# Kernel tuning notes

Measured on AMD Instinct MI355X. Metric: run time of the kernel, lower is better.

Reference implementation:

```python
import jax, jax.numpy as jnp
import numpy as np

HEAD = 8
KERNEL = 7


def setup_inputs() -> dict:
    key = jax.random.key(0)
    ks = jax.random.split(key, 5)
    N, C, H, W = 2, 256, 56, 56
    scale = 1.0 / np.sqrt(C)
    queries = jax.random.normal(ks[0], (N, C, H, W), jnp.float32)
    key_t = jax.random.normal(ks[1], (N, C, H, W), jnp.float32)
    in_proj_w = jax.random.normal(ks[2], (3 * C, C), jnp.float32) * scale
    in_proj_b = jnp.zeros((3 * C,), jnp.float32)
    out_proj_w = jax.random.normal(ks[3], (C, C), jnp.float32) * scale
    out_proj_b = jnp.zeros((C,), jnp.float32)
    pos_enc = jnp.full((1, 1), float(KERNEL ** 2), jnp.float32)  # nn.Parameter([[kernel**2]])
    return dict(queries=queries, key=key_t, pos_enc=pos_enc,
                in_proj_w=in_proj_w, in_proj_b=in_proj_b,
                out_proj_w=out_proj_w, out_proj_b=out_proj_b)


def reference(queries, key, pos_enc, in_proj_w, in_proj_b, out_proj_w, out_proj_b):
    N, C, H, W = queries.shape
    k2 = KERNEL * KERNEL
    c = (KERNEL - 1) // 2
    # zero-pad key and extract k x k neighborhoods (same ordering as unfold: row-major i*k+j)
    kp = jnp.pad(key, ((0, 0), (0, 0), (c, c), (c, c)))
    patches = jnp.stack([kp[:, :, i:i + H, j:j + W]
                         for i in range(KERNEL) for j in range(KERNEL)], axis=-1)  # (N,C,H,W,k2)
    kv = patches.reshape(N, C, H * W, k2) + pos_enc[0, 0]   # scalar position bias
    kv = kv.transpose(0, 2, 3, 1)                            # (N, P, k2, C), P = H*W pixels
    q = queries.reshape(N, C, H * W).transpose(0, 2, 1)      # (N, P, C)

    Wq, Wk, Wv = jnp.split(in_proj_w, 3, axis=0)
    bq, bk, bv = jnp.split(in_proj_b, 3)
    d = C // HEAD
    qh = (q @ Wq.T + bq).reshape(N, H * W, HEAD, d)
    kh = (kv @ Wk.T + bk).reshape(N, H * W, k2, HEAD, d)
    vh = (kv @ Wv.T + bv).reshape(N, H * W, k2, HEAD, d)

    scores = jnp.einsum('nphd,npkhd->nphk', qh, kh) / jnp.sqrt(jnp.asarray(d, qh.dtype))
    attn = jax.nn.softmax(scores, axis=-1)
    o = jnp.einsum('nphk,npkhd->nphd', attn, vh).reshape(N, H * W, C)
    out = o @ out_proj_w.T + out_proj_b                       # (N, P, C)
    return out.transpose(0, 2, 1).reshape(N, C, H, W)
```

## Files before the change

kernel.cpp:

```cpp
#include <hip/hip_runtime.h>
#include <stdint.h>

#define HW 56
#define P 3136
#define C 256
#define CP (C*P)

typedef float  f32x4  __attribute__((ext_vector_type(4)));
typedef short  short8 __attribute__((ext_vector_type(8)));

__device__ __forceinline__ unsigned short f2bf(float f) {
    uint32_t u = __float_as_uint(f);
    uint32_t r = (u + 0x7fffu + ((u >> 16) & 1u)) >> 16;
    return (unsigned short)r;
}
__device__ __forceinline__ float bl(uint32_t u) { return __uint_as_float(u << 16); }
__device__ __forceinline__ float bh(uint32_t u) { return __uint_as_float(u & 0xffff0000u); }

__device__ __forceinline__ void gload16(const void* g, const void* l) {
    __builtin_amdgcn_global_load_lds(
        (const __attribute__((address_space(1))) uint32_t*)g,
        (__attribute__((address_space(3))) uint32_t*)l, 16, 0, 0);
}

__global__ __launch_bounds__(256) void wconv_vb_kernel(const float* __restrict__ ipw,
                                                       const float* __restrict__ opw,
                                                       const float* __restrict__ ipb,
                                                       const float* __restrict__ pos,
                                                       unsigned short* __restrict__ Wb,
                                                       float* __restrict__ vbc) {
    int bx = blockIdx.x;
    if (bx < 256) {
        int i4 = bx * 256 + threadIdx.x;
        const float4* src = (i4 < 49152) ? (const float4*)ipw : (const float4*)opw;
        int idx = (i4 < 49152) ? i4 : i4 - 49152;
        float4 v = src[idx];
        ((ushort4*)Wb)[i4] = make_ushort4(f2bf(v.x), f2bf(v.y), f2bf(v.z), f2bf(v.w));
    } else {
        int b = bx - 256;
        int w = threadIdx.x >> 6, lane = threadIdx.x & 63;
        float pe = pos[0];
        #pragma unroll
        for (int i = 0; i < 4; ++i) {
            int r = b * 16 + w * 4 + i;
            const float* row = ipw + (size_t)(512 + r) * 256;
            float s = row[lane] + row[lane + 64] + row[lane + 128] + row[lane + 192];
            #pragma unroll
            for (int off = 32; off; off >>= 1) s += __shfl_xor(s, off);
            if (lane == 0) vbc[r] = fmaf(pe, s, ipb[512 + r]);
        }
    }
}

__global__ __launch_bounds__(256) void tconv_kernel(const float* __restrict__ queries,
                                                    const float* __restrict__ key,
                                                    unsigned short* __restrict__ Qt,
                                                    unsigned short* __restrict__ Kt) {
    __shared__ float Ls[64][65];
    int t = threadIdx.x;
    int p0 = blockIdx.x * 64, ci0 = blockIdx.y * 64;
    int n = blockIdx.z & 1, which = blockIdx.z >> 1;
    const float* X = (which ? key : queries) + (size_t)n * CP;
    unsigned short* Xt = (which ? Kt : Qt) + (size_t)n * P * 256;

    int c = t & 63, r0 = t >> 6;
    #pragma unroll
    for (int rr = 0; rr < 16; ++rr) {
        int cil = r0 * 16 + rr;
        Ls[c][cil] = X[(size_t)(ci0 + cil) * P + p0 + c];
    }
    __syncthreads();
    int pl = t >> 2, cch = (t & 3) * 16;
    uint32_t us[8];
    #pragma unroll
    for (int j = 0; j < 8; ++j) {
        float lo = Ls[pl][cch + 2 * j], hi = Ls[pl][cch + 2 * j + 1];
        us[j] = (uint32_t)f2bf(lo) | ((uint32_t)f2bf(hi) << 16);
    }
    uint4* dst = (uint4*)(Xt + (size_t)(p0 + pl) * 256 + ci0 + cch);
    dst[0] = make_uint4(us[0], us[1], us[2], us[3]);
    dst[1] = make_uint4(us[4], us[5], us[6], us[7]);
}

__device__ __forceinline__ void gemm_core(const unsigned short* __restrict__ A,
                                          const unsigned short* __restrict__ B,
                                          int p0, unsigned short* As, unsigned short* Bs,
                                          f32x4 acc[4][2]) {
    int tid = threadIdx.x;
    int wid = __builtin_amdgcn_readfirstlane(tid >> 6);
    int lane = tid & 63;
    int wr = wid >> 1, wc = wid & 1;

    #pragma unroll
    for (int m = 0; m < 4; ++m)
        #pragma unroll
        for (int j = 0; j < 2; ++j) acc[m][j] = (f32x4){0.f, 0.f, 0.f, 0.f};

    for (int k0 = 0; k0 < 256; k0 += 32) {
        #pragma unroll
        for (int i = 0; i < 2; ++i) {
            int ch = i * 256 + (wid << 6) + lane;
            int row = ch >> 2;
            int g = (ch & 3) ^ ((row >> 1) & 3);
            gload16(A + (size_t)row * 256 + k0 + g * 8, (const char*)As + i * 4096 + wid * 1024);
        }
        {
            int ch = (wid << 6) + lane;
            int row = ch >> 2;
            int g = (ch & 3) ^ ((row >> 1) & 3);
            gload16(B + (size_t)(p0 + row) * 256 + k0 + g * 8, (const char*)Bs + wid * 1024);
        }
        __syncthreads();
        short8 af[4], bfr[2];
        #pragma unroll
        for (int m = 0; m < 4; ++m) {
            int col = (wr << 6) + m * 16 + (lane & 15);
            int phys = (lane >> 4) ^ ((col >> 1) & 3);
            af[m] = *(const short8*)((const char*)As + col * 64 + phys * 16);
        }
        #pragma unroll
        for (int j = 0; j < 2; ++j) {
            int pl = (wc << 5) + j * 16 + (lane & 15);
            int phys = (lane >> 4) ^ ((pl >> 1) & 3);
            bfr[j] = *(const short8*)((const char*)Bs + pl * 64 + phys * 16);
        }
        #pragma unroll
        for (int m = 0; m < 4; ++m)
            #pragma unroll
            for (int j = 0; j < 2; ++j)
                acc[m][j] = __builtin_amdgcn_mfma_f32_16x16x32_bf16(af[m], bfr[j], acc[m][j], 0, 0, 0);
        __syncthreads();
    }
}

__global__ __launch_bounds__(256) void proj_mfma(const unsigned short* __restrict__ Wb,
                                                 const unsigned short* __restrict__ Qt,
                                                 const unsigned short* __restrict__ Kt,
                                                 const float* __restrict__ ipb,
                                                 unsigned short* __restrict__ Qb,
                                                 unsigned short* __restrict__ Kb,
                                                 unsigned short* __restrict__ Vb) {
    __shared__ __align__(16) unsigned short As[4096];
    __shared__ __align__(16) unsigned short Bs[2048];
    int ty = blockIdx.y, n = blockIdx.z;
    int p0 = blockIdx.x * 64;
    int proj = ty >> 1;
    int co0 = ty * 128;
    const unsigned short* A = Wb + (size_t)co0 * 256;
    const unsigned short* B = (proj == 0 ? Qt : Kt) + (size_t)n * P * 256;
    unsigned short* outb = (proj == 0 ? Qb : (proj == 1 ? Kb : Vb)) + (size_t)n * 8 * P * 32;
    int col0 = (ty & 1) * 128;

    f32x4 acc[4][2];
    gemm_core(A, B, p0, As, Bs, acc);

    int lane = threadIdx.x & 63;
    int wid = threadIdx.x >> 6;
    int wr = wid >> 1, wc = wid & 1;
    #pragma unroll
    for (int m = 0; m < 4; ++m)
        #pragma unroll
        for (int j = 0; j < 2; ++j) {
            int col = col0 + (wr << 6) + m * 16 + (lane >> 4) * 4;
            int p   = p0 + (wc << 5) + j * 16 + (lane & 15);
            float v0 = acc[m][j][0], v1 = acc[m][j][1], v2 = acc[m][j][2], v3 = acc[m][j][3];
            if (proj == 0) {
                int cg = co0 + (wr << 6) + m * 16 + (lane >> 4) * 4;
                v0 += ipb[cg]; v1 += ipb[cg + 1]; v2 += ipb[cg + 2]; v3 += ipb[cg + 3];
            }
            int h = col >> 5, d = col & 31;
            ushort4 u = make_ushort4(f2bf(v0), f2bf(v1), f2bf(v2), f2bf(v3));
            *(ushort4*)(outb + ((size_t)(h * P + p)) * 32 + d) = u;
        }
}

__constant__ const float kScale = 0.17677669529663687f;

template<int T0, int T1>
__device__ __forceinline__ void tap_range(const float* __restrict__ q,
                                          const unsigned short* __restrict__ Kbase,
                                          int p, int y, int x,
                                          float* __restrict__ ws_col, float& l) {
    #pragma unroll
    for (int t = T0; t < T1; ++t) {
        int dy = t / 7 - 3, dx = t % 7 - 3;
        int yy = y + dy, xx = x + dx;
        bool in = (yy >= 0) & (yy < HW) & (xx >= 0) & (xx < HW);
        int pnb = in ? (p + dy * HW + dx) : p;
        const uint4* kr = (const uint4*)(Kbase + (size_t)pnb * 32);
        float dot = 0.f;
        #pragma unroll
        for (int c = 0; c < 4; ++c) {
            uint4 u = kr[c];
            dot = fmaf(q[c*8+0], bl(u.x), dot); dot = fmaf(q[c*8+1], bh(u.x), dot);
            dot = fmaf(q[c*8+2], bl(u.y), dot); dot = fmaf(q[c*8+3], bh(u.y), dot);
            dot = fmaf(q[c*8+4], bl(u.z), dot); dot = fmaf(q[c*8+5], bh(u.z), dot);
            dot = fmaf(q[c*8+6], bl(u.w), dot); dot = fmaf(q[c*8+7], bh(u.w), dot);
        }
        float e = in ? __expf(dot * kScale) : 0.f;
        l += in ? e : 1.0f;
        ws_col[t * 64] = e;
    }
}

__global__ __launch_bounds__(256) void attn_kernel(const unsigned short* __restrict__ Qb,
                                                   const unsigned short* __restrict__ Kb,
                                                   const unsigned short* __restrict__ Vb,
                                                   unsigned short* __restrict__ Ot) {
    __shared__ float Ws[49][64];
    __shared__ float Lp[4][64];
    int tid = threadIdx.x;
    int lane = tid & 63, wave = tid >> 6;
    int p = blockIdx.x * 64 + lane;
    int h = blockIdx.y, n = blockIdx.z;
    int y = p / HW, x = p % HW;

    const unsigned short* Kbase = Kb + (size_t)(n * 8 + h) * P * 32;
    const unsigned short* Vbase = Vb + (size_t)(n * 8 + h) * P * 32;

    const uint4* qr = (const uint4*)(Qb + ((size_t)((n * 8 + h) * P + p)) * 32);
    float q[32];
    #pragma unroll
    for (int c = 0; c < 4; ++c) {
        uint4 u = qr[c];
        q[c*8+0] = bl(u.x); q[c*8+1] = bh(u.x); q[c*8+2] = bl(u.y); q[c*8+3] = bh(u.y);
        q[c*8+4] = bl(u.z); q[c*8+5] = bh(u.z); q[c*8+6] = bl(u.w); q[c*8+7] = bh(u.w);
    }

    float l = 0.f;
    float* ws_col = &Ws[0][lane];
    if      (wave == 0) tap_range< 0, 13>(q, Kbase, p, y, x, ws_col, l);
    else if (wave == 1) tap_range<13, 25>(q, Kbase, p, y, x, ws_col, l);
    else if (wave == 2) tap_range<25, 37>(q, Kbase, p, y, x, ws_col, l);
    else                tap_range<37, 49>(q, Kbase, p, y, x, ws_col, l);
    Lp[wave][lane] = l;
    __syncthreads();

    float lt = Lp[0][lane] + Lp[1][lane] + Lp[2][lane] + Lp[3][lane];
    float inv = __builtin_amdgcn_rcpf(lt);

    int d0 = wave * 8;
    float o[8] = {0.f, 0.f, 0.f, 0.f, 0.f, 0.f, 0.f, 0.f};
    #pragma unroll
    for (int t = 0; t < 49; ++t) {
        int dy = t / 7 - 3, dx = t % 7 - 3;
        int yy = y + dy, xx = x + dx;
        bool in = (yy >= 0) & (yy < HW) & (xx >= 0) & (xx < HW);
        int pnb = in ? (p + dy * HW + dx) : p;
        float w = Ws[t][lane];
        uint4 u = *(const uint4*)(Vbase + (size_t)pnb * 32 + d0);
        o[0] = fmaf(w, bl(u.x), o[0]); o[1] = fmaf(w, bh(u.x), o[1]);
        o[2] = fmaf(w, bl(u.y), o[2]); o[3] = fmaf(w, bh(u.y), o[3]);
        o[4] = fmaf(w, bl(u.z), o[4]); o[5] = fmaf(w, bh(u.z), o[5]);
        o[6] = fmaf(w, bl(u.w), o[6]); o[7] = fmaf(w, bh(u.w), o[7]);
    }
    uint32_t us[4];
    #pragma unroll
    for (int j = 0; j < 4; ++j)
        us[j] = (uint32_t)f2bf(o[2*j] * inv) | ((uint32_t)f2bf(o[2*j+1] * inv) << 16);
    *(uint4*)(Ot + (size_t)(n * P + p) * 256 + h * 32 + d0) =
        make_uint4(us[0], us[1], us[2], us[3]);
}

__global__ __launch_bounds__(256) void outproj_mfma(const unsigned short* __restrict__ Wb,
                                                    const unsigned short* __restrict__ Ot,
                                                    const float* __restrict__ opw,
                                                    const float* __restrict__ opb,
                                                    const float* __restrict__ vbc,
                                                    float* __restrict__ out) {
    __shared__ __align__(16) unsigned short As[4096];
    __shared__ __align__(16) unsigned short Bs[2048];
    __shared__ float obc_s[128];
    int tid = threadIdx.x;
    int n = blockIdx.z;
    int p0 = blockIdx.x * 64;
    int co0 = blockIdx.y * 128;

    {
        int r = tid >> 1, half = tid & 1;
        const float* row = opw + (size_t)(co0 + r) * 256 + half * 128;
        const float* vh = vbc + half * 128;
        float s = 0.f;
        #pragma unroll 8
        for (int i = 0; i < 128; ++i) s = fmaf(row[i], vh[i], s);
        s += __shfl_xor(s, 1);
        if (half == 0) obc_s[r] = s + opb[co0 + r];
    }

    const unsigned short* A = Wb + (size_t)(768 + co0) * 256;
    const unsigned short* B = Ot + (size_t)n * P * 256;
    f32x4 acc[4][2];
    gemm_core(A, B, p0, As, Bs, acc);

    int lane = tid & 63;
    int wid = tid >> 6;
    int wr = wid >> 1, wc = wid & 1;
    #pragma unroll
    for (int m = 0; m < 4; ++m)
        #pragma unroll
        for (int j = 0; j < 2; ++j) {
            int col = (wr << 6) + m * 16 + (lane >> 4) * 4;
            int p  = p0 + (wc << 5) + j * 16 + (lane & 15);
            #pragma unroll
            for (int i = 0; i < 4; ++i)
                out[(size_t)n * CP + (size_t)(co0 + col + i) * P + p] = acc[m][j][i] + obc_s[col + i];
        }
}

extern "C" void kernel_launch(void* const* d_in, const int* in_sizes, int n_in,
                              void* d_out, int out_size, void* d_ws, size_t ws_size,
                              hipStream_t stream) {
    (void)in_sizes; (void)n_in; (void)out_size; (void)ws_size;
    const float* queries = (const float*)d_in[0];
    const float* key     = (const float*)d_in[1];
    const float* pos     = (const float*)d_in[2];
    const float* ipw     = (const float*)d_in[3];
    const float* ipb     = (const float*)d_in[4];
    const float* opw     = (const float*)d_in[5];
    const float* opb     = (const float*)d_in[6];
    float* out = (float*)d_out;

    unsigned short* us = (unsigned short*)d_ws;
    const size_t SZ = (size_t)2 * P * 256;
    unsigned short* Qt = us;
    unsigned short* Kt = us + SZ;
    unsigned short* Qb = us + 2 * SZ;
    unsigned short* Kb = us + 3 * SZ;
    unsigned short* Vb = us + 4 * SZ;
    unsigned short* Ot = us + 5 * SZ;
    unsigned short* Wb = us + 6 * SZ;
    float* vbc = (float*)(us + 6 * SZ + 262144);

    hipLaunchKernelGGL(wconv_vb_kernel, dim3(272), dim3(256), 0, stream,
                       ipw, opw, ipb, pos, Wb, vbc);
    hipLaunchKernelGGL(tconv_kernel, dim3(49, 4, 4), dim3(256), 0, stream,
                       queries, key, Qt, Kt);
    hipLaunchKernelGGL(proj_mfma, dim3(49, 6, 2), dim3(256), 0, stream,
                       Wb, Qt, Kt, ipb, Qb, Kb, Vb);
    hipLaunchKernelGGL(attn_kernel, dim3(49, 8, 2), dim3(256), 0, stream, Qb, Kb, Vb, Ot);
    hipLaunchKernelGGL(outproj_mfma, dim3(49, 2, 2), dim3(256), 0, stream,
                       Wb, Ot, opw, opb, vbc, out);
}
```

Baseline: 126.5 us.

## Merge prep kernels, deepen GEMM K-step to 64, shrink outproj tile

Folds the weight-conversion and transpose-convert kernels into a single prep launch, removing one kernel launch and its serialization. The shared GEMM core now loads K=64 per iteration with an 8-way XOR swizzle, halving the number of barrier pairs per tile. The output projection uses 64-row output tiles instead of 128, doubling its block count for better CU occupancy on a small grid. This costs more LDS per block in the projection kernel and more redundant bias-vector work in outproj.

Result: faster. 122.0 us, median of 2 (-3.6%).

```diff
diff --git a/kernel.cpp b/kernel.cpp
--- a/kernel.cpp
+++ b/kernel.cpp
@@ -23,12 +23,17 @@
         (__attribute__((address_space(3))) uint32_t*)l, 16, 0, 0);
 }
 
-__global__ __launch_bounds__(256) void wconv_vb_kernel(const float* __restrict__ ipw,
-                                                       const float* __restrict__ opw,
-                                                       const float* __restrict__ ipb,
-                                                       const float* __restrict__ pos,
-                                                       unsigned short* __restrict__ Wb,
-                                                       float* __restrict__ vbc) {
+__global__ __launch_bounds__(256) void prep_kernel(const float* __restrict__ queries,
+                                                   const float* __restrict__ key,
+                                                   const float* __restrict__ ipw,
+                                                   const float* __restrict__ opw,
+                                                   const float* __restrict__ ipb,
+                                                   const float* __restrict__ pos,
+                                                   unsigned short* __restrict__ Wb,
+                                                   float* __restrict__ vbc,
+                                                   unsigned short* __restrict__ Qt,
+                                                   unsigned short* __restrict__ Kt) {
+    __shared__ float Ls[64][65];
     int bx = blockIdx.x;
     if (bx < 256) {
         int i4 = bx * 256 + threadIdx.x;
@@ -36,7 +41,7 @@
         int idx = (i4 < 49152) ? i4 : i4 - 49152;
         float4 v = src[idx];
         ((ushort4*)Wb)[i4] = make_ushort4(f2bf(v.x), f2bf(v.y), f2bf(v.z), f2bf(v.w));
-    } else {
+    } else if (bx < 272) {
         int b = bx - 256;
         int w = threadIdx.x >> 6, lane = threadIdx.x & 63;
         float pe = pos[0];
@@ -49,86 +54,92 @@
             for (int off = 32; off; off >>= 1) s += __shfl_xor(s, off);
             if (lane == 0) vbc[r] = fmaf(pe, s, ipb[512 + r]);
         }
-    }
-}
-
-__global__ __launch_bounds__(256) void tconv_kernel(const float* __restrict__ queries,
-                                                    const float* __restrict__ key,
-                                                    unsigned short* __restrict__ Qt,
-                                                    unsigned short* __restrict__ Kt) {
-    __shared__ float Ls[64][65];
-    int t = threadIdx.x;
-    int p0 = blockIdx.x * 64, ci0 = blockIdx.y * 64;
-    int n = blockIdx.z & 1, which = blockIdx.z >> 1;
-    const float* X = (which ? key : queries) + (size_t)n * CP;
-    unsigned short* Xt = (which ? Kt : Qt) + (size_t)n * P * 256;
-
-    int c = t & 63, r0 = t >> 6;
-    #pragma unroll
-    for (int rr = 0; rr < 16; ++rr) {
-        int cil = r0 * 16 + rr;
-        Ls[c][cil] = X[(size_t)(ci0 + cil) * P + p0 + c];
-    }
-    __syncthreads();
-    int pl = t >> 2, cch = (t & 3) * 16;
-    uint32_t us[8];
-    #pragma unroll
-    for (int j = 0; j < 8; ++j) {
-        float lo = Ls[pl][cch + 2 * j], hi = Ls[pl][cch + 2 * j + 1];
-        us[j] = (uint32_t)f2bf(lo) | ((uint32_t)f2bf(hi) << 16);
-    }
-    uint4* dst = (uint4*)(Xt + (size_t)(p0 + pl) * 256 + ci0 + cch);
-    dst[0] = make_uint4(us[0], us[1], us[2], us[3]);
-    dst[1] = make_uint4(us[4], us[5], us[6], us[7]);
-}
-
-__device__ __forceinline__ void gemm_core(const unsigned short* __restrict__ A,
-                                          const unsigned short* __restrict__ B,
-                                          int p0, unsigned short* As, unsigned short* Bs,
-                                          f32x4 acc[4][2]) {
+    } else {
+        int idx = bx - 272;
+        int t = threadIdx.x;
+        int p0 = (idx % 49) * 64, ci0 = ((idx / 49) & 3) * 64;
+        int z = idx / 196;
+        int n = z & 1, which = z >> 1;
+        const float* X = (which ? key : queries) + (size_t)n * CP;
+        unsigned short* Xt = (which ? Kt : Qt) + (size_t)n * P * 256;
+
+        int c = t & 63, r0 = t >> 6;
+        #pragma unroll
+        for (int rr = 0; rr < 16; ++rr) {
+            int cil = r0 * 16 + rr;
+            Ls[c][cil] = X[(size_t)(ci0 + cil) * P + p0 + c];
+        }
+        __syncthreads();
+        int pl = t >> 2, cch = (t & 3) * 16;
+        uint32_t us[8];
+        #pragma unroll
+        for (int j = 0; j < 8; ++j) {
+            float lo = Ls[pl][cch + 2 * j], hi = Ls[pl][cch + 2 * j + 1];
+            us[j] = (uint32_t)f2bf(lo) | ((uint32_t)f2bf(hi) << 16);
+        }
+        uint4* dst = (uint4*)(Xt + (size_t)(p0 + pl) * 256 + ci0 + cch);
+        dst[0] = make_uint4(us[0], us[1], us[2], us[3]);
+        dst[1] = make_uint4(us[4], us[5], us[6], us[7]);
+    }
+}
+
+template<int MR>
+__device__ __forceinline__ void gemm_core64(const unsigned short* __restrict__ A,
+                                            const unsigned short* __restrict__ B,
+                                            int p0, unsigned short* As, unsigned short* Bs,
+                                            f32x4 acc[MR][2]) {
     int tid = threadIdx.x;
     int wid = __builtin_amdgcn_readfirstlane(tid >> 6);
     int lane = tid & 63;
     int wr = wid >> 1, wc = wid & 1;
 
     #pragma unroll
-    for (int m = 0; m < 4; ++m)
+    for (int m = 0; m < MR; ++m)
         #pragma unroll
         for (int j = 0; j < 2; ++j) acc[m][j] = (f32x4){0.f, 0.f, 0.f, 0.f};
 
-    for (int k0 = 0; k0 < 256; k0 += 32) {
+    for (int k0 = 0; k0 < 256; k0 += 64) {
+        #pragma unroll
+        for (int i = 0; i < MR; ++i) {
+            int ch = i * 256 + (wid << 6) + lane;
+            int row = ch >> 3;
+            int g = (ch & 7) ^ (row & 7);
+            gload16(A + (size_t)row * 256 + k0 + g * 8,
+                    (const char*)As + (i * 256 + (wid << 6)) * 16);
+        }
         #pragma unroll
         for (int i = 0; i < 2; ++i) {
             int ch = i * 256 + (wid << 6) + lane;
-            int row = ch >> 2;
-            int g = (ch & 3) ^ ((row >> 1) & 3);
-            gload16(A + (size_t)row * 256 + k0 + g * 8, (const char*)As + i * 4096 + wid * 1024);
-        }
-        {
-            int ch = (wid << 6) + lane;
-            int row = ch >> 2;
-            int g = (ch & 3) ^ ((row >> 1) & 3);
-            gload16(B + (size_t)(p0 + row) * 256 + k0 + g * 8, (const char*)Bs + wid * 1024);
+            int row = ch >> 3;
+            int g = (ch & 7) ^ (row & 7);
+            gload16(B + (size_t)(p0 + row) * 256 + k0 + g * 8,
+                    (const char*)Bs + (i * 256 + (wid << 6)) * 16);
         }
         __syncthreads();
-        short8 af[4], bfr[2];
-        #pragma unroll
-        for (int m = 0; m < 4; ++m) {
-            int col = (wr << 6) + m * 16 + (lane & 15);
-            int phys = (lane >> 4) ^ ((col >> 1) & 3);
-            af[m] = *(const short8*)((const char*)As + col * 64 + phys * 16);
-        }
-        #pragma unroll
-        for (int j = 0; j < 2; ++j) {
-            int pl = (wc << 5) + j * 16 + (lane & 15);
-            int phys = (lane >> 4) ^ ((pl >> 1) & 3);
-            bfr[j] = *(const short8*)((const char*)Bs + pl * 64 + phys * 16);
-        }
-        #pragma unroll
-        for (int m = 0; m < 4; ++m)
+        short8 af[MR][2], bfr[2][2];
+        #pragma unroll
+        for (int m = 0; m < MR; ++m)
+            #pragma unroll
+            for (int ks = 0; ks < 2; ++ks) {
+                int col = wr * (MR * 16) + m * 16 + (lane & 15);
+                int phys = (ks * 4 + (lane >> 4)) ^ (col & 7);
+                af[m][ks] = *(const short8*)((const char*)As + col * 128 + phys * 16);
+            }
+        #pragma unroll
+        for (int j = 0; j < 2; ++j)
+            #pragma unroll
+            for (int ks = 0; ks < 2; ++ks) {
+                int pl = (wc << 5) + j * 16 + (lane & 15);
+                int phys = (ks * 4 + (lane >> 4)) ^ (pl & 7);
+                bfr[j][ks] = *(const short8*)((const char*)Bs + pl * 128 + phys * 16);
+            }
+        #pragma unroll
+        for (int m = 0; m < MR; ++m)
             #pragma unroll
             for (int j = 0; j < 2; ++j)
-                acc[m][j] = __builtin_amdgcn_mfma_f32_16x16x32_bf16(af[m], bfr[j], acc[m][j], 0, 0, 0);
+                #pragma unroll
+                for (int ks = 0; ks < 2; ++ks)
+                    acc[m][j] = __builtin_amdgcn_mfma_f32_16x16x32_bf16(af[m][ks], bfr[j][ks], acc[m][j], 0, 0, 0);
         __syncthreads();
     }
 }
@@ -140,8 +151,8 @@
                                                  unsigned short* __restrict__ Qb,
                                                  unsigned short* __restrict__ Kb,
                                                  unsigned short* __restrict__ Vb) {
-    __shared__ __align__(16) unsigned short As[4096];
-    __shared__ __align__(16) unsigned short Bs[2048];
+    __shared__ __align__(16) unsigned short As[8192];
+    __shared__ __align__(16) unsigned short Bs[4096];
     int ty = blockIdx.y, n = blockIdx.z;
     int p0 = blockIdx.x * 64;
     int proj = ty >> 1;
@@ -152,7 +163,7 @@
     int col0 = (ty & 1) * 128;
 
     f32x4 acc[4][2];
-    gemm_core(A, B, p0, As, Bs, acc);
+    gemm_core64<4>(A, B, p0, As, Bs, acc);
 
     int lane = threadIdx.x & 63;
     int wid = threadIdx.x >> 6;
@@ -269,37 +280,38 @@
                                                     const float* __restrict__ vbc,
                                                     float* __restrict__ out) {
     __shared__ __align__(16) unsigned short As[4096];
-    __shared__ __align__(16) unsigned short Bs[2048];
-    __shared__ float obc_s[128];
+    __shared__ __align__(16) unsigned short Bs[4096];
+    __shared__ float obc_s[64];
     int tid = threadIdx.x;
     int n = blockIdx.z;
     int p0 = blockIdx.x * 64;
-    int co0 = blockIdx.y * 128;
+    int co0 = blockIdx.y * 64;
 
     {
-        int r = tid >> 1, half = tid & 1;
-        const float* row = opw + (size_t)(co0 + r) * 256 + half * 128;
-        const float* vh = vbc + half * 128;
+        int r = tid >> 2, qq = tid & 3;
+        const float* row = opw + (size_t)(co0 + r) * 256 + qq * 64;
+        const float* vh = vbc + qq * 64;
         float s = 0.f;
         #pragma unroll 8
-        for (int i = 0; i < 128; ++i) s = fmaf(row[i], vh[i], s);
+        for (int i = 0; i < 64; ++i) s = fmaf(row[i], vh[i], s);
         s += __shfl_xor(s, 1);
-        if (half == 0) obc_s[r] = s + opb[co0 + r];
+        s += __shfl_xor(s, 2);
+        if (qq == 0) obc_s[r] = s + opb[co0 + r];
     }
 
     const unsigned short* A = Wb + (size_t)(768 + co0) * 256;
     const unsigned short* B = Ot + (size_t)n * P * 256;
-    f32x4 acc[4][2];
-    gemm_core(A, B, p0, As, Bs, acc);
+    f32x4 acc[2][2];
+    gemm_core64<2>(A, B, p0, As, Bs, acc);
 
     int lane = tid & 63;
     int wid = tid >> 6;
     int wr = wid >> 1, wc = wid & 1;
     #pragma unroll
-    for (int m = 0; m < 4; ++m)
+    for (int m = 0; m < 2; ++m)
         #pragma unroll
         for (int j = 0; j < 2; ++j) {
-            int col = (wr << 6) + m * 16 + (lane >> 4) * 4;
+            int col = (wr << 5) + m * 16 + (lane >> 4) * 4;
             int p  = p0 + (wc << 5) + j * 16 + (lane & 15);
             #pragma unroll
             for (int i = 0; i < 4; ++i)
@@ -331,13 +343,11 @@
     unsigned short* Wb = us + 6 * SZ;
     float* vbc = (float*)(us + 6 * SZ + 262144);
 
-    hipLaunchKernelGGL(wconv_vb_kernel, dim3(272), dim3(256), 0, stream,
-                       ipw, opw, ipb, pos, Wb, vbc);
-    hipLaunchKernelGGL(tconv_kernel, dim3(49, 4, 4), dim3(256), 0, stream,
-                       queries, key, Qt, Kt);
+    hipLaunchKernelGGL(prep_kernel, dim3(1056), dim3(256), 0, stream,
+                       queries, key, ipw, opw, ipb, pos, Wb, vbc, Qt, Kt);
     hipLaunchKernelGGL(proj_mfma, dim3(49, 6, 2), dim3(256), 0, stream,
                        Wb, Qt, Kt, ipb, Qb, Kb, Vb);
     hipLaunchKernelGGL(attn_kernel, dim3(49, 8, 2), dim3(256), 0, stream, Qb, Kb, Vb, Ot);
-    hipLaunchKernelGGL(outproj_mfma, dim3(49, 2, 2), dim3(256), 0, stream,
+    hipLaunchKernelGGL(outproj_mfma, dim3(49, 4, 2), dim3(256), 0, stream,
                        Wb, Ot, opw, opb, vbc, out);
 }
```
